# Performance work log

Hardware: AMD Instinct MI355X
Metric: run time of the kernel (lower is better)

## Reference

```python
import jax, jax.numpy as jnp
import numpy as np

B, O, I = 128, 1024, 1024
EPS = 1e-07

def setup_inputs() -> dict:
    key = jax.random.key(0)
    ks = jax.random.split(key, 7)
    data = jax.random.normal(ks[0], (B, I), dtype=jnp.float32)
    # parameters, matching torch init: 2*rand-1, rand+0.1, 2*rand-1, ones+0.1, rand, rand
    input_x = 2.0 * jax.random.uniform(ks[1], (1, O, I), dtype=jnp.float32) - 1.0
    input_y = jax.random.uniform(ks[2], (1, O, I), dtype=jnp.float32) + 0.1
    output_x = 2.0 * jax.random.uniform(ks[3], (1, O, I), dtype=jnp.float32) - 1.0
    output_y = jnp.ones((1, O, I), dtype=jnp.float32) + 0.1
    linkage_add = jax.random.uniform(ks[4], (1, O, I), dtype=jnp.float32)
    linkage_mul = jax.random.uniform(ks[5], (1, O, I), dtype=jnp.float32)
    return {"data": data, "input_x": input_x, "input_y": input_y,
            "output_x": output_x, "output_y": output_y,
            "linkage_add": linkage_add, "linkage_mul": linkage_mul}

def reference(data, input_x, input_y, output_x, output_y, linkage_add, linkage_mul):
    shape = data.shape
    d = data.reshape(-1, 1, I)                      # (B,1,I)
    inp = input_x / input_y                          # (1,O,I)
    out = output_x / output_y                        # (1,O,I)
    tests = (inp + linkage_add) * (1.0 + linkage_mul)
    error = (tests - out) * jax.nn.sigmoid(d)        # (B,O,I)
    w = jax.nn.softmax(1.0 / jnp.sqrt(error * error + EPS), axis=1)
    expect = d * w                                   # (B,O,I)
    return jnp.sum(expect, axis=2).reshape(shape)
```

## Files before the change

kernel.cpp:

```cpp
#include <hip/hip_runtime.h>

#define B_ 128
#define O_ 1024
#define I_ 1024
#define NCHUNK 64
#define CI (I_ / NCHUNK)
#define WPB 4
#define TT_BYTES ((size_t)O_ * I_ * sizeof(float))

#define LOG2E_F  1.4426950408889634f
#define LN2_F    0.6931471805599453f
#define LN2SQ_F  0.4804530139182014f
#define EPSC_F   (1e-7f * LN2SQ_F)

typedef float v2f __attribute__((ext_vector_type(2)));

__device__ __forceinline__ float fast_rsq(float x)  { return __builtin_amdgcn_rsqf(x); }
__device__ __forceinline__ float fast_exp2(float x) { return __builtin_amdgcn_exp2f(x); }
__device__ __forceinline__ float fast_rcp(float x)  { return __builtin_amdgcn_rcpf(x); }

__device__ __forceinline__ float rfl(float x) {
    return __builtin_bit_cast(float,
        __builtin_amdgcn_readfirstlane(__builtin_bit_cast(int, x)));
}

template <int CTRL>
__device__ __forceinline__ float dpp_add(float v) {
    int x = __builtin_amdgcn_update_dpp(0, __builtin_bit_cast(int, v),
                                        CTRL, 0xf, 0xf, true);
    return v + __builtin_bit_cast(float, x);
}
__device__ __forceinline__ float wave_sum_uniform(float v) {
    v = dpp_add<0xB1>(v);
    v = dpp_add<0x4E>(v);
    v = dpp_add<0x141>(v);
    v = dpp_add<0x140>(v);
    v = dpp_add<0x142>(v);
    v = dpp_add<0x143>(v);
    return __builtin_bit_cast(float,
        __builtin_amdgcn_readlane(__builtin_bit_cast(int, v), 63));
}

__global__ __launch_bounds__(256) void build_T2_kernel(
    const float* __restrict__ ix, const float* __restrict__ iy,
    const float* __restrict__ ox, const float* __restrict__ oy,
    const float* __restrict__ la, const float* __restrict__ lm,
    float* __restrict__ Tt2, unsigned* __restrict__ minbits,
    float* __restrict__ out_zero)
{
    __shared__ float tile[32][33];
    __shared__ unsigned mloc[32];
    const int i0 = blockIdx.x * 32;
    const int o0 = blockIdx.y * 32;
    const int tx = threadIdx.x;
    const int ty = threadIdx.y;
    const int t  = ty * 32 + tx;

    if (t < 32) mloc[t] = 0xFFFFFFFFu;

    const int bid = blockIdx.y * gridDim.x + blockIdx.x;
    if (t < 128) out_zero[bid * 128 + t] = 0.0f;

#pragma unroll
    for (int r = 0; r < 32; r += 8) {
        const int o = o0 + ty + r;
        const int i = i0 + tx;
        const int idx = o * I_ + i;
        const float tt = fmaf(ix[idx] * fast_rcp(iy[idx]) + la[idx],
                              1.0f + lm[idx],
                              -(ox[idx] * fast_rcp(oy[idx])));
        tile[ty + r][tx] = tt * tt;
    }
    __syncthreads();
#pragma unroll
    for (int r = 0; r < 32; r += 8) {
        const int i = i0 + ty + r;
        const int o = o0 + tx;
        Tt2[i * O_ + o] = tile[tx][ty + r];
    }
    const int il = t & 31;
    const int g  = t >> 5;
    float mn = fminf(fminf(tile[4 * g + 0][il], tile[4 * g + 1][il]),
                     fminf(tile[4 * g + 2][il], tile[4 * g + 3][il]));
    atomicMin(&mloc[il], __builtin_bit_cast(unsigned, mn));
    __syncthreads();
    if (t < 32) atomicMin(&minbits[i0 + t], mloc[t]);
}

__global__ __launch_bounds__(256) void aeg_main_kernel(
    const float* __restrict__ data,
    const float* __restrict__ Tt2,
    const float* __restrict__ minr2,
    float* __restrict__ out)
{
    __shared__ float red[WPB][O_];

    const int w    = threadIdx.x >> 6;
    const int lane = threadIdx.x & 63;
    const int chunk = blockIdx.x * WPB + w;
    const int b     = blockIdx.y;

    const float4* rowbase = (const float4*)(Tt2 + (size_t)chunk * CI * O_);

    const float4* dv4 = (const float4*)(data + b * I_ + chunk * CI);
    const float4* mr4 = (const float4*)(minr2 + chunk * CI);
    float dvf[CI], mrf[CI];
#pragma unroll
    for (int k = 0; k < 4; ++k) {
        const float4 a = dv4[k];
        const float4 m = mr4[k];
        dvf[4 * k + 0] = a.x; dvf[4 * k + 1] = a.y;
        dvf[4 * k + 2] = a.z; dvf[4 * k + 3] = a.w;
        mrf[4 * k + 0] = m.x; mrf[4 * k + 1] = m.y;
        mrf[4 * k + 2] = m.z; mrf[4 * k + 3] = m.w;
    }
    float sdv[CI], ss2[CI], sm2[CI];
#pragma unroll
    for (int j = 0; j < CI; ++j) {
        const float dv  = dvf[j];
        const float sig = fast_rcp(1.0f + fast_exp2(-dv * LOG2E_F));
        const float sc  = sig * LN2_F;
        const float s2  = sc * sc;
        const float m2  = fast_rsq(fmaf(mrf[j], s2, EPSC_F));
        sdv[j] = rfl(dv);
        ss2[j] = rfl(s2);
        sm2[j] = rfl(m2);
    }

    v2f acc2[8];
#pragma unroll
    for (int j = 0; j < 8; ++j) acc2[j] = (v2f)0.0f;

    float4 rr[2][4];
#pragma unroll
    for (int k = 0; k < 4; ++k) rr[0][k] = rowbase[lane + 64 * k];

#pragma unroll
    for (int ii = 0; ii < CI; ++ii) {
        if (ii + 1 < CI) {
            const float4* nrow = rowbase + (size_t)(ii + 1) * (O_ / 4);
#pragma unroll
            for (int k = 0; k < 4; ++k) rr[(ii + 1) & 1][k] = nrow[lane + 64 * k];
        }
        const float4* r = rr[ii & 1];
        const v2f s2v = {ss2[ii], ss2[ii]};
        const v2f m2v = {sm2[ii], sm2[ii]};
        const v2f epv = {EPSC_F, EPSC_F};

        v2f e2[8];
        v2f zv0 = (v2f)0.0f, zv1 = (v2f)0.0f;
#pragma unroll
        for (int k = 0; k < 4; ++k) {
            const v2f a = {r[k].x, r[k].y};
            const v2f c = {r[k].z, r[k].w};
            const v2f q0 = a * s2v + epv;
            const v2f q1 = c * s2v + epv;
            v2f t0, t1;
            t0.x = fast_rsq(q0.x); t0.y = fast_rsq(q0.y);
            t1.x = fast_rsq(q1.x); t1.y = fast_rsq(q1.y);
            t0 -= m2v;
            t1 -= m2v;
            v2f ev0, ev1;
            ev0.x = fast_exp2(t0.x); ev0.y = fast_exp2(t0.y);
            ev1.x = fast_exp2(t1.x); ev1.y = fast_exp2(t1.y);
            e2[2 * k]     = ev0;
            e2[2 * k + 1] = ev1;
            zv0 += ev0;
            zv1 += ev1;
        }
        const v2f zv = zv0 + zv1;
        const float zt = wave_sum_uniform(zv.x + zv.y);
        const float scale = sdv[ii] * fast_rcp(zt);
        const v2f sc2 = {scale, scale};
#pragma unroll
        for (int j = 0; j < 8; ++j)
            acc2[j] = e2[j] * sc2 + acc2[j];
    }

#pragma unroll
    for (int k = 0; k < 4; ++k) {
        float4 v;
        v.x = acc2[2 * k].x;     v.y = acc2[2 * k].y;
        v.z = acc2[2 * k + 1].x; v.w = acc2[2 * k + 1].y;
        ((float4*)&red[w][256 * k])[lane] = v;
    }
    __syncthreads();

    const int t = threadIdx.x;
    float4 v = ((const float4*)red[0])[t];
#pragma unroll
    for (int ww = 1; ww < WPB; ++ww) {
        const float4 u = ((const float4*)red[ww])[t];
        v.x += u.x; v.y += u.y; v.z += u.z; v.w += u.w;
    }
    float* ob = out + b * O_ + 4 * t;
    atomicAdd(&ob[0], v.x);
    atomicAdd(&ob[1], v.y);
    atomicAdd(&ob[2], v.z);
    atomicAdd(&ob[3], v.w);
}

extern "C" void kernel_launch(void* const* d_in, const int* in_sizes, int n_in,
                              void* d_out, int out_size, void* d_ws, size_t ws_size,
                              hipStream_t stream)
{
    const float* data = (const float*)d_in[0];
    const float* ix   = (const float*)d_in[1];
    const float* iy   = (const float*)d_in[2];
    const float* ox   = (const float*)d_in[3];
    const float* oy   = (const float*)d_in[4];
    const float* la   = (const float*)d_in[5];
    const float* lm   = (const float*)d_in[6];
    float* out  = (float*)d_out;
    float* Tt2  = (float*)d_ws;
    unsigned* minbits = (unsigned*)((char*)d_ws + TT_BYTES);

    (void)hipMemsetAsync(minbits, 0xFF, I_ * sizeof(unsigned), stream);

    build_T2_kernel<<<dim3(I_ / 32, O_ / 32), dim3(32, 8), 0, stream>>>(
        ix, iy, ox, oy, la, lm, Tt2, minbits, out);

    aeg_main_kernel<<<dim3(NCHUNK / WPB, B_), 256, 0, stream>>>(
        data, Tt2, (const float*)minbits, out);
}
```

Baseline: 122.1 us.

## Compute per-column scalars lane-parallel, drop manual double buffer, raise occupancy hint

Each lane now computes the sigmoid and min-based scale for one of the 16 input columns, and the results are broadcast with readlane. Before, every lane redundantly computed all 16 and used readfirstlane. The explicit register double-buffering of Tt2 rows is removed in favour of a plain per-iteration load, leaving load scheduling to the compiler. Launch bounds now request 8 blocks per CU. Together these cut VGPR pressure so more waves stay resident to hide memory latency, at the risk of losing the explicit prefetch overlap.

```diff
diff --git a/kernel.cpp b/kernel.cpp
--- a/kernel.cpp
+++ b/kernel.cpp
@@ -19,9 +19,9 @@
 __device__ __forceinline__ float fast_exp2(float x) { return __builtin_amdgcn_exp2f(x); }
 __device__ __forceinline__ float fast_rcp(float x)  { return __builtin_amdgcn_rcpf(x); }
 
-__device__ __forceinline__ float rfl(float x) {
+__device__ __forceinline__ float readlane_f(float x, int l) {
     return __builtin_bit_cast(float,
-        __builtin_amdgcn_readfirstlane(__builtin_bit_cast(int, x)));
+        __builtin_amdgcn_readlane(__builtin_bit_cast(int, x), l));
 }
 
 template <int CTRL>
@@ -87,7 +87,7 @@
     if (t < 32) atomicMin(&minbits[i0 + t], mloc[t]);
 }
 
-__global__ __launch_bounds__(256) void aeg_main_kernel(
+__global__ __launch_bounds__(256, 8) void aeg_main_kernel(
     const float* __restrict__ data,
     const float* __restrict__ Tt2,
     const float* __restrict__ minr2,
@@ -102,47 +102,33 @@
 
     const float4* rowbase = (const float4*)(Tt2 + (size_t)chunk * CI * O_);
 
-    const float4* dv4 = (const float4*)(data + b * I_ + chunk * CI);
-    const float4* mr4 = (const float4*)(minr2 + chunk * CI);
-    float dvf[CI], mrf[CI];
-#pragma unroll
-    for (int k = 0; k < 4; ++k) {
-        const float4 a = dv4[k];
-        const float4 m = mr4[k];
-        dvf[4 * k + 0] = a.x; dvf[4 * k + 1] = a.y;
-        dvf[4 * k + 2] = a.z; dvf[4 * k + 3] = a.w;
-        mrf[4 * k + 0] = m.x; mrf[4 * k + 1] = m.y;
-        mrf[4 * k + 2] = m.z; mrf[4 * k + 3] = m.w;
-    }
+    const int li = lane & 15;
+    const float dv_l = data[b * I_ + chunk * CI + li];
+    const float mr_l = minr2[chunk * CI + li];
+    const float sig_l = fast_rcp(1.0f + fast_exp2(-dv_l * LOG2E_F));
+    const float sc_l  = sig_l * LN2_F;
+    const float s2_l  = sc_l * sc_l;
+    const float m2_l  = fast_rsq(fmaf(mr_l, s2_l, EPSC_F));
+
     float sdv[CI], ss2[CI], sm2[CI];
 #pragma unroll
     for (int j = 0; j < CI; ++j) {
-        const float dv  = dvf[j];
-        const float sig = fast_rcp(1.0f + fast_exp2(-dv * LOG2E_F));
-        const float sc  = sig * LN2_F;
-        const float s2  = sc * sc;
-        const float m2  = fast_rsq(fmaf(mrf[j], s2, EPSC_F));
-        sdv[j] = rfl(dv);
-        ss2[j] = rfl(s2);
-        sm2[j] = rfl(m2);
+        sdv[j] = readlane_f(dv_l, j);
+        ss2[j] = readlane_f(s2_l, j);
+        sm2[j] = readlane_f(m2_l, j);
     }
 
     v2f acc2[8];
 #pragma unroll
     for (int j = 0; j < 8; ++j) acc2[j] = (v2f)0.0f;
 
-    float4 rr[2][4];
-#pragma unroll
-    for (int k = 0; k < 4; ++k) rr[0][k] = rowbase[lane + 64 * k];
-
 #pragma unroll
     for (int ii = 0; ii < CI; ++ii) {
-        if (ii + 1 < CI) {
-            const float4* nrow = rowbase + (size_t)(ii + 1) * (O_ / 4);
-#pragma unroll
-            for (int k = 0; k < 4; ++k) rr[(ii + 1) & 1][k] = nrow[lane + 64 * k];
-        }
-        const float4* r = rr[ii & 1];
+        const float4* r4 = rowbase + (size_t)ii * (O_ / 4);
+        float4 rr[4];
+#pragma unroll
+        for (int k = 0; k < 4; ++k) rr[k] = r4[lane + 64 * k];
+
         const v2f s2v = {ss2[ii], ss2[ii]};
         const v2f m2v = {sm2[ii], sm2[ii]};
         const v2f epv = {EPSC_F, EPSC_F};
@@ -151,8 +137,8 @@
         v2f zv0 = (v2f)0.0f, zv1 = (v2f)0.0f;
 #pragma unroll
         for (int k = 0; k < 4; ++k) {
-            const v2f a = {r[k].x, r[k].y};
-            const v2f c = {r[k].z, r[k].w};
+            const v2f a = {rr[k].x, rr[k].y};
+            const v2f c = {rr[k].z, rr[k].w};
             const v2f q0 = a * s2v + epv;
             const v2f q1 = c * s2v + epv;
             v2f t0, t1;
```

Measured after the change: 155.1 us. 1.27x slower.
